# Kernel tuning notes

Hardware: AMD Instinct MI355X
Metric: run time of the kernel (lower is better)

Reference implementation:

```python
import jax, jax.numpy as jnp
import numpy as np

NUM_RADIAL = 6
HIDDEN = 128
OUT_EMB = 256
OUT_CH = 128
NUM_LAYERS = 3
E = 1600000
N_NODES = 50000


def setup_inputs() -> dict:
    key = jax.random.key(0)
    ks = jax.random.split(key, 16)
    inp = {
        "x": jax.random.normal(ks[0], (E, HIDDEN), dtype=jnp.float32),
        "rbf": jax.random.normal(ks[1], (E, NUM_RADIAL), dtype=jnp.float32),
        "idx_i": jax.random.randint(ks[2], (E,), 0, N_NODES, dtype=jnp.int32),
        "num_nodes": N_NODES,
        # torch nn.Linear weights are [out, in]
        "W_basis": jax.random.normal(ks[3], (HIDDEN, NUM_RADIAL), dtype=jnp.float32) * 0.3,
        "W_proj": jax.random.normal(ks[4], (OUT_EMB, HIDDEN), dtype=jnp.float32) * 0.08,
        "W_final": jax.random.normal(ks[5], (OUT_CH, OUT_EMB), dtype=jnp.float32) * 0.06,
    }
    for l in range(NUM_LAYERS):
        inp[f"W{l}"] = jax.random.normal(ks[6 + 2 * l], (OUT_EMB, OUT_EMB), dtype=jnp.float32) * 0.06
        inp[f"b{l}"] = jnp.zeros((OUT_EMB,), dtype=jnp.float32)
    return inp


def reference(x, rbf, idx_i, num_nodes, W_basis, W_proj, W_final, W0, b0, W1, b1, W2, b2):
    # basis_transformation: [E, num_radial] -> [E, hidden]
    basis = rbf @ W_basis.T
    # elementwise mul then edge->node scatter-sum
    msg = basis * x                                  # [E, hidden]
    agg = jax.ops.segment_sum(msg, idx_i, num_segments=num_nodes)  # [N, hidden]
    # output_projection (no bias)
    h = agg @ W_proj.T                                # [N, out_emb]
    for W, b in ((W0, b0), (W1, b1), (W2, b2)):
        h = jax.nn.silu(h @ W.T + b)
    return h @ W_final.T                              # [N, out_channels]
```

## Files before the change

kernel.cpp:

```cpp
#include <hip/hip_runtime.h>

typedef float f4 __attribute__((ext_vector_type(4)));
typedef float f2 __attribute__((ext_vector_type(2)));
typedef int   i4 __attribute__((ext_vector_type(4)));
typedef short bf16x8 __attribute__((ext_vector_type(8)));
typedef unsigned short u16x8 __attribute__((ext_vector_type(8)));
typedef unsigned short u16x4 __attribute__((ext_vector_type(4)));
typedef float f32x4 __attribute__((ext_vector_type(4)));

constexpr int HIDDEN     = 128;
constexpr int OUT_EMB    = 256;
constexpr int OUT_CH     = 128;
constexpr int NUM_RADIAL = 6;
constexpr int NBLK       = 128;

constexpr int OFF_Wp = 0;
constexpr int OFF_W0 = OFF_Wp + 256 * 128;
constexpr int OFF_W1 = OFF_W0 + 256 * 256;
constexpr int OFF_W2 = OFF_W1 + 256 * 256;
constexpr int OFF_Wf = OFF_W2 + 256 * 256;
constexpr int WTOT   = OFF_Wf + 128 * 256;

__device__ __forceinline__ unsigned short f2bf(float f) {
    unsigned int u = __float_as_uint(f);
    return (unsigned short)((u + 0x7FFFu + ((u >> 16) & 1u)) >> 16);
}
__device__ __forceinline__ float bf2f(unsigned short h) {
    return __uint_as_float(((unsigned int)h) << 16);
}

__global__ __launch_bounds__(256) void prep_kernel(
    const float* __restrict__ Wp, const float* __restrict__ W0,
    const float* __restrict__ W1, const float* __restrict__ W2,
    const float* __restrict__ Wf,
    unsigned short* __restrict__ whi, unsigned short* __restrict__ wlo,
    int* __restrict__ count, int N)
{
    const int i = blockIdx.x * 256 + threadIdx.x;
    if (i < N) count[i] = 0;
    if (i < WTOT) {
        const float* src; int off;
        if      (i < OFF_W0) { src = Wp; off = i - OFF_Wp; }
        else if (i < OFF_W1) { src = W0; off = i - OFF_W0; }
        else if (i < OFF_W2) { src = W1; off = i - OFF_W1; }
        else if (i < OFF_Wf) { src = W2; off = i - OFF_W2; }
        else                 { src = Wf; off = i - OFF_Wf; }
        float v = src[off];
        unsigned short h = f2bf(v);
        whi[i] = h;
        wlo[i] = f2bf(v - bf2f(h));
    }
}

__global__ __launch_bounds__(256) void hist_kernel(const int* __restrict__ idx,
                                                   int* __restrict__ count, long E)
{
    long i = ((long)blockIdx.x * blockDim.x + threadIdx.x) * 4;
    if (i + 3 < E) {
        i4 v = *(const i4*)(idx + i);
#pragma unroll
        for (int k = 0; k < 4; ++k) atomicAdd(&count[v[k]], 1);
    } else {
        for (long t = i; t < E; ++t) atomicAdd(&count[idx[t]], 1);
    }
}

__global__ __launch_bounds__(1024) void scan_kernel(const int* __restrict__ count,
                                                    int* __restrict__ start,
                                                    int* __restrict__ cursor, int N)
{
    __shared__ int part[1024];
    const int tid   = threadIdx.x;
    const int chunk = (N + 1023) / 1024;
    const int lo    = tid * chunk;
    const int hi    = min(lo + chunk, N);

    int s = 0;
    for (int i = lo; i < hi; ++i) s += count[i];
    part[tid] = s;
    __syncthreads();

    for (int off = 1; off < 1024; off <<= 1) {
        int v = part[tid];
        int u = (tid >= off) ? part[tid - off] : 0;
        __syncthreads();
        part[tid] = v + u;
        __syncthreads();
    }

    int run = (tid > 0) ? part[tid - 1] : 0;
    for (int i = lo; i < hi; ++i) {
        start[i]  = run;
        cursor[i] = run;
        run += count[i];
    }
    if (tid == 1023) start[N] = part[1023];
}

__global__ __launch_bounds__(256) void scatter_perm_kernel(const int* __restrict__ idx,
                                                           int* __restrict__ cursor,
                                                           int* __restrict__ perm, long E)
{
    long i = ((long)blockIdx.x * blockDim.x + threadIdx.x) * 4;
    if (i + 3 < E) {
        i4 v = *(const i4*)(idx + i);
#pragma unroll
        for (int k = 0; k < 4; ++k) {
            int p = atomicAdd(&cursor[v[k]], 1);
            perm[p] = (int)(i + k);
        }
    } else {
        for (long t = i; t < E; ++t) {
            int p = atomicAdd(&cursor[idx[t]], 1);
            perm[p] = (int)t;
        }
    }
}

__device__ __forceinline__ void edge_accum(const float* __restrict__ x,
                                           const float* __restrict__ rbf,
                                           const float wb[4][NUM_RADIAL],
                                           int e, int l, f4& acc)
{
    const float* rp = rbf + (long)e * NUM_RADIAL;
    f2 r01 = *(const f2*)(rp);
    f2 r23 = *(const f2*)(rp + 2);
    f2 r45 = *(const f2*)(rp + 4);
    f4 xv  = *(const f4*)(x + (long)e * HIDDEN + 4 * l);
    float rb[NUM_RADIAL] = {r01[0], r01[1], r23[0], r23[1], r45[0], r45[1]};
#pragma unroll
    for (int c = 0; c < 4; ++c) {
        float b = 0.f;
#pragma unroll
        for (int r = 0; r < NUM_RADIAL; ++r) b = __builtin_fmaf(rb[r], wb[c][r], b);
        acc[c] = __builtin_fmaf(b, xv[c], acc[c]);
    }
}

__global__ __launch_bounds__(256) void gather_kernel(
    const float* __restrict__ x, const float* __restrict__ rbf,
    const float* __restrict__ Wb, const int* __restrict__ perm,
    const int* __restrict__ start, unsigned short* __restrict__ aggb, int N)
{
    const int lane = threadIdx.x & 63;
    const int half = lane >> 5;
    const int l    = lane & 31;
    const int wid  = threadIdx.x >> 6;
    const int node = blockIdx.x * 4 + wid;
    if (node >= N) return;

    float wb[4][NUM_RADIAL];
#pragma unroll
    for (int c = 0; c < 4; ++c)
#pragma unroll
        for (int r = 0; r < NUM_RADIAL; ++r)
            wb[c][r] = Wb[(4 * l + c) * NUM_RADIAL + r];

    const int j0 = start[node], j1 = start[node + 1];
    f4 acc = {0.f, 0.f, 0.f, 0.f};

    int j = j0 + half;
    for (; j + 6 < j1; j += 8) {
        const int e0 = perm[j];
        const int e1 = perm[j + 2];
        const int e2 = perm[j + 4];
        const int e3 = perm[j + 6];
        edge_accum(x, rbf, wb, e0, l, acc);
        edge_accum(x, rbf, wb, e1, l, acc);
        edge_accum(x, rbf, wb, e2, l, acc);
        edge_accum(x, rbf, wb, e3, l, acc);
    }
    for (; j < j1; j += 2) edge_accum(x, rbf, wb, perm[j], l, acc);

#pragma unroll
    for (int c = 0; c < 4; ++c) acc[c] += __shfl_xor(acc[c], 32);

    if (half == 0) {
        u16x4 o;
#pragma unroll
        for (int c = 0; c < 4; ++c) o[c] = f2bf(acc[c]);
        *(u16x4*)(aggb + (long)node * HIDDEN + 4 * l) = o;
    }
}

__device__ __forceinline__ int swz(int node, int col) {
    return (node * 256 + col) ^ ((node & 7) << 3);
}

template <int IN, int OUT, bool BIAS_ACT, bool LAST>
__device__ __forceinline__ void mfma_layer(
    const unsigned short* __restrict__ whi, const unsigned short* __restrict__ wlo,
    const float* __restrict__ bias,
    unsigned short* H, float* __restrict__ outp,
    int node0, int N, int wm, int wn, int lane)
{
    const int lr = lane & 15;
    const int lg = lane >> 4;
    constexpr int NT = OUT / 64;
    const int wbase = wn * (OUT / 4);
    const int mrow0 = wm * 64;

    f32x4 acc[4][NT];
#pragma unroll
    for (int nt = 0; nt < NT; ++nt) {
        float bb = 0.f;
        if constexpr (BIAS_ACT) bb = bias[wbase + nt * 16 + lr];
#pragma unroll
        for (int mt = 0; mt < 4; ++mt) {
            acc[mt][nt][0] = bb; acc[mt][nt][1] = bb;
            acc[mt][nt][2] = bb; acc[mt][nt][3] = bb;
        }
    }

    for (int ks = 0; ks < IN / 32; ++ks) {
        const int k0 = ks * 32 + lg * 8;
        bf16x8 ah[4];
#pragma unroll
        for (int mt = 0; mt < 4; ++mt)
            ah[mt] = *(const bf16x8*)&H[swz(mrow0 + mt * 16 + lr, k0)];
#pragma unroll
        for (int nt = 0; nt < NT; ++nt) {
            const long wrow = (long)(wbase + nt * 16 + lr) * IN + k0;
            bf16x8 bh = *(const bf16x8*)&whi[wrow];
            bf16x8 bl = *(const bf16x8*)&wlo[wrow];
#pragma unroll
            for (int mt = 0; mt < 4; ++mt) {
                acc[mt][nt] = __builtin_amdgcn_mfma_f32_16x16x32_bf16(ah[mt], bh, acc[mt][nt], 0, 0, 0);
                acc[mt][nt] = __builtin_amdgcn_mfma_f32_16x16x32_bf16(ah[mt], bl, acc[mt][nt], 0, 0, 0);
            }
        }
    }

    __syncthreads();

#pragma unroll
    for (int mt = 0; mt < 4; ++mt) {
#pragma unroll
        for (int nt = 0; nt < NT; ++nt) {
#pragma unroll
            for (int r = 0; r < 4; ++r) {
                float v = acc[mt][nt][r];
                if constexpr (BIAS_ACT) v = v / (1.f + __expf(-v));
                const int node = mrow0 + mt * 16 + lg * 4 + r;
                const int col  = wbase + nt * 16 + lr;
                if constexpr (LAST) {
                    if (node0 + node < N) outp[(long)(node0 + node) * OUT + col] = v;
                } else {
                    H[swz(node, col)] = f2bf(v);
                }
            }
        }
    }
    if constexpr (!LAST) __syncthreads();
}

__global__ __launch_bounds__(512, 4) void node_mlp_mfma_kernel(
    const unsigned short* __restrict__ aggb,
    const unsigned short* __restrict__ whi, const unsigned short* __restrict__ wlo,
    const float* __restrict__ b0, const float* __restrict__ b1,
    const float* __restrict__ b2,
    float* __restrict__ out, int N)
{
    __shared__ unsigned short H[NBLK * 256];

    const int tid   = threadIdx.x;
    const int w     = tid >> 6;
    const int lane  = tid & 63;
    const int wm    = w >> 2;
    const int wn    = w & 3;
    const int node0 = blockIdx.x * NBLK;

#pragma unroll
    for (int i = 0; i < (NBLK * HIDDEN) / (512 * 8); ++i) {
        const int e    = (i * 512 + tid) * 8;
        const int node = e >> 7;
        const int col  = e & 127;
        u16x8 v = {0, 0, 0, 0, 0, 0, 0, 0};
        if (node0 + node < N) v = *(const u16x8*)(aggb + (long)(node0 + node) * HIDDEN + col);
        *(u16x8*)&H[swz(node, col)] = v;
    }
    __syncthreads();

    mfma_layer<HIDDEN,  OUT_EMB, false, false>(whi + OFF_Wp, wlo + OFF_Wp, nullptr, H, nullptr, node0, N, wm, wn, lane);
    mfma_layer<OUT_EMB, OUT_EMB, true,  false>(whi + OFF_W0, wlo + OFF_W0, b0,      H, nullptr, node0, N, wm, wn, lane);
    mfma_layer<OUT_EMB, OUT_EMB, true,  false>(whi + OFF_W1, wlo + OFF_W1, b1,      H, nullptr, node0, N, wm, wn, lane);
    mfma_layer<OUT_EMB, OUT_EMB, true,  false>(whi + OFF_W2, wlo + OFF_W2, b2,      H, nullptr, node0, N, wm, wn, lane);
    mfma_layer<OUT_EMB, OUT_CH,  false, true >(whi + OFF_Wf, wlo + OFF_Wf, nullptr, H, out,     node0, N, wm, wn, lane);
}

extern "C" void kernel_launch(void* const* d_in, const int* in_sizes, int n_in,
                              void* d_out, int out_size, void* d_ws, size_t ws_size,
                              hipStream_t stream)
{
    const float* x   = (const float*)d_in[0];
    const float* rbf = (const float*)d_in[1];
    const int*   idx = (const int*)d_in[2];
    const float* Wb  = (const float*)d_in[4];
    const float* Wp  = (const float*)d_in[5];
    const float* Wf  = (const float*)d_in[6];
    const float* W0  = (const float*)d_in[7];
    const float* b0  = (const float*)d_in[8];
    const float* W1  = (const float*)d_in[9];
    const float* b1  = (const float*)d_in[10];
    const float* W2  = (const float*)d_in[11];
    const float* b2  = (const float*)d_in[12];

    const long E = (long)in_sizes[0] / HIDDEN;
    const int  N = out_size / OUT_CH;

    unsigned short* aggb = (unsigned short*)d_ws;
    int* count  = (int*)(aggb + (long)N * HIDDEN);
    int* startp = count + N;
    int* cursor = startp + N + 1;
    int* perm   = cursor + N;
    uintptr_t p = (uintptr_t)(perm + E);
    p = (p + 15) & ~(uintptr_t)15;
    unsigned short* whi = (unsigned short*)p;
    unsigned short* wlo = whi + WTOT;

    const int pb = (max((int)WTOT, N) + 255) / 256;
    prep_kernel<<<pb, 256, 0, stream>>>(Wp, W0, W1, W2, Wf, whi, wlo, count, N);

    const long Eq = (E + 3) / 4;
    const int eb = (int)((Eq + 255) / 256);
    hist_kernel<<<eb, 256, 0, stream>>>(idx, count, E);
    scan_kernel<<<1, 1024, 0, stream>>>(count, startp, cursor, N);
    scatter_perm_kernel<<<eb, 256, 0, stream>>>(idx, cursor, perm, E);
    gather_kernel<<<(N + 3) / 4, 256, 0, stream>>>(x, rbf, Wb, perm, startp, aggb, N);

    node_mlp_mfma_kernel<<<(N + NBLK - 1) / NBLK, 512, 0, stream>>>(
        aggb, whi, wlo, b0, b1, b2, (float*)d_out, N);
}
```

Before: 702.6 us.

## Parallelize prefix scan across blocks and make gather kernel persistent

Replaces the single-block 1024-thread serial-chunk scan with a three-kernel multi-block scan (block sums, scan of block sums, per-block scan and write). Converts the gather kernel to a grid-stride persistent form with a fixed 2048 blocks and an occupancy hint, so the Wb weights are loaded once per wave instead of once per node. The single-block scan was latency-bound with long serial loops per thread. The new scan supports at most 256 blocks (65536 nodes). The fixed gather grid may balance load worse across nodes with different degrees.

Result: faster. 611.5 us (-13.0%).

```diff
diff --git a/kernel.cpp b/kernel.cpp
--- a/kernel.cpp
+++ b/kernel.cpp
@@ -65,36 +65,63 @@
     }
 }
 
-__global__ __launch_bounds__(1024) void scan_kernel(const int* __restrict__ count,
-                                                    int* __restrict__ start,
-                                                    int* __restrict__ cursor, int N)
-{
-    __shared__ int part[1024];
-    const int tid   = threadIdx.x;
-    const int chunk = (N + 1023) / 1024;
-    const int lo    = tid * chunk;
-    const int hi    = min(lo + chunk, N);
-
-    int s = 0;
-    for (int i = lo; i < hi; ++i) s += count[i];
-    part[tid] = s;
-    __syncthreads();
-
-    for (int off = 1; off < 1024; off <<= 1) {
-        int v = part[tid];
-        int u = (tid >= off) ? part[tid - off] : 0;
+__global__ __launch_bounds__(256) void scan_bsum_kernel(const int* __restrict__ count,
+                                                        int* __restrict__ bsum, int N)
+{
+    __shared__ int red[4];
+    const int i = blockIdx.x * 256 + threadIdx.x;
+    int v = (i < N) ? count[i] : 0;
+#pragma unroll
+    for (int off = 1; off < 64; off <<= 1) v += __shfl_xor(v, off);
+    if ((threadIdx.x & 63) == 0) red[threadIdx.x >> 6] = v;
+    __syncthreads();
+    if (threadIdx.x == 0) bsum[blockIdx.x] = red[0] + red[1] + red[2] + red[3];
+}
+
+__global__ __launch_bounds__(256) void scan_base_kernel(const int* __restrict__ bsum,
+                                                        int* __restrict__ bbase,
+                                                        int* __restrict__ start,
+                                                        int nb, int N, int E)
+{
+    __shared__ int s[256];
+    const int t = threadIdx.x;
+    int v = (t < nb) ? bsum[t] : 0;
+    s[t] = v;
+    __syncthreads();
+    for (int off = 1; off < 256; off <<= 1) {
+        int a = s[t];
+        int b = (t >= off) ? s[t - off] : 0;
         __syncthreads();
-        part[tid] = v + u;
+        s[t] = a + b;
         __syncthreads();
     }
-
-    int run = (tid > 0) ? part[tid - 1] : 0;
-    for (int i = lo; i < hi; ++i) {
-        start[i]  = run;
-        cursor[i] = run;
-        run += count[i];
-    }
-    if (tid == 1023) start[N] = part[1023];
+    if (t < nb) bbase[t] = s[t] - v;
+    if (t == 0) start[N] = E;
+}
+
+__global__ __launch_bounds__(256) void scan_write_kernel(const int* __restrict__ count,
+                                                         const int* __restrict__ bbase,
+                                                         int* __restrict__ start,
+                                                         int* __restrict__ cursor, int N)
+{
+    __shared__ int s[256];
+    const int t = threadIdx.x;
+    const int i = blockIdx.x * 256 + t;
+    int v = (i < N) ? count[i] : 0;
+    s[t] = v;
+    __syncthreads();
+    for (int off = 1; off < 256; off <<= 1) {
+        int a = s[t];
+        int b = (t >= off) ? s[t - off] : 0;
+        __syncthreads();
+        s[t] = a + b;
+        __syncthreads();
+    }
+    if (i < N) {
+        int sv = bbase[blockIdx.x] + s[t] - v;
+        start[i]  = sv;
+        cursor[i] = sv;
+    }
 }
 
 __global__ __launch_bounds__(256) void scatter_perm_kernel(const int* __restrict__ idx,
@@ -137,17 +164,16 @@
     }
 }
 
-__global__ __launch_bounds__(256) void gather_kernel(
+__global__ __launch_bounds__(256, 6) void gather_kernel(
     const float* __restrict__ x, const float* __restrict__ rbf,
     const float* __restrict__ Wb, const int* __restrict__ perm,
-    const int* __restrict__ start, unsigned short* __restrict__ aggb, int N)
+    const int* __restrict__ start, unsigned short* __restrict__ aggb,
+    int N, int nwaves)
 {
     const int lane = threadIdx.x & 63;
     const int half = lane >> 5;
     const int l    = lane & 31;
-    const int wid  = threadIdx.x >> 6;
-    const int node = blockIdx.x * 4 + wid;
-    if (node >= N) return;
+    const int wgid = blockIdx.x * (blockDim.x >> 6) + (threadIdx.x >> 6);
 
     float wb[4][NUM_RADIAL];
 #pragma unroll
@@ -156,30 +182,32 @@
         for (int r = 0; r < NUM_RADIAL; ++r)
             wb[c][r] = Wb[(4 * l + c) * NUM_RADIAL + r];
 
-    const int j0 = start[node], j1 = start[node + 1];
-    f4 acc = {0.f, 0.f, 0.f, 0.f};
-
-    int j = j0 + half;
-    for (; j + 6 < j1; j += 8) {
-        const int e0 = perm[j];
-        const int e1 = perm[j + 2];
-        const int e2 = perm[j + 4];
-        const int e3 = perm[j + 6];
-        edge_accum(x, rbf, wb, e0, l, acc);
-        edge_accum(x, rbf, wb, e1, l, acc);
-        edge_accum(x, rbf, wb, e2, l, acc);
-        edge_accum(x, rbf, wb, e3, l, acc);
-    }
-    for (; j < j1; j += 2) edge_accum(x, rbf, wb, perm[j], l, acc);
-
-#pragma unroll
-    for (int c = 0; c < 4; ++c) acc[c] += __shfl_xor(acc[c], 32);
-
-    if (half == 0) {
-        u16x4 o;
-#pragma unroll
-        for (int c = 0; c < 4; ++c) o[c] = f2bf(acc[c]);
-        *(u16x4*)(aggb + (long)node * HIDDEN + 4 * l) = o;
+    for (int node = wgid; node < N; node += nwaves) {
+        const int j0 = start[node], j1 = start[node + 1];
+        f4 acc = {0.f, 0.f, 0.f, 0.f};
+
+        int j = j0 + half;
+        for (; j + 6 < j1; j += 8) {
+            const int e0 = perm[j];
+            const int e1 = perm[j + 2];
+            const int e2 = perm[j + 4];
+            const int e3 = perm[j + 6];
+            edge_accum(x, rbf, wb, e0, l, acc);
+            edge_accum(x, rbf, wb, e1, l, acc);
+            edge_accum(x, rbf, wb, e2, l, acc);
+            edge_accum(x, rbf, wb, e3, l, acc);
+        }
+        for (; j < j1; j += 2) edge_accum(x, rbf, wb, perm[j], l, acc);
+
+#pragma unroll
+        for (int c = 0; c < 4; ++c) acc[c] += __shfl_xor(acc[c], 32);
+
+        if (half == 0) {
+            u16x4 o;
+#pragma unroll
+            for (int c = 0; c < 4; ++c) o[c] = f2bf(acc[c]);
+            *(u16x4*)(aggb + (long)node * HIDDEN + 4 * l) = o;
+        }
     }
 }
 
@@ -307,12 +335,15 @@
 
     const long E = (long)in_sizes[0] / HIDDEN;
     const int  N = out_size / OUT_CH;
+    const int  nb = (N + 255) / 256;
 
     unsigned short* aggb = (unsigned short*)d_ws;
     int* count  = (int*)(aggb + (long)N * HIDDEN);
     int* startp = count + N;
     int* cursor = startp + N + 1;
-    int* perm   = cursor + N;
+    int* bsum   = cursor + N;
+    int* bbase  = bsum + nb;
+    int* perm   = bbase + nb;
     uintptr_t p = (uintptr_t)(perm + E);
     p = (p + 15) & ~(uintptr_t)15;
     unsigned short* whi = (unsigned short*)p;
@@ -324,9 +355,16 @@
     const long Eq = (E + 3) / 4;
     const int eb = (int)((Eq + 255) / 256);
     hist_kernel<<<eb, 256, 0, stream>>>(idx, count, E);
-    scan_kernel<<<1, 1024, 0, stream>>>(count, startp, cursor, N);
+
+    scan_bsum_kernel<<<nb, 256, 0, stream>>>(count, bsum, N);
+    scan_base_kernel<<<1, 256, 0, stream>>>(bsum, bbase, startp, nb, N, (int)E);
+    scan_write_kernel<<<nb, 256, 0, stream>>>(count, bbase, startp, cursor, N);
+
     scatter_perm_kernel<<<eb, 256, 0, stream>>>(idx, cursor, perm, E);
-    gather_kernel<<<(N + 3) / 4, 256, 0, stream>>>(x, rbf, Wb, perm, startp, aggb, N);
+
+    const int gblocks = 2048;
+    const int nwaves  = gblocks * 4;
+    gather_kernel<<<gblocks, 256, 0, stream>>>(x, rbf, Wb, perm, startp, aggb, N, nwaves);
 
     node_mlp_mfma_kernel<<<(N + NBLK - 1) / NBLK, 512, 0, stream>>>(
         aggb, whi, wlo, b0, b1, b2, (float*)d_out, N);
```
